# Kernel optimization log

Measured on AMD Instinct MI355X. Metric: run time of the kernel, lower is better.

Reference implementation:

```python
import jax, jax.numpy as jnp
import numpy as np


def setup_inputs() -> dict:
    key = jax.random.key(0)
    ks = jax.random.split(key, 6)
    B, L, H = 32, 2048, 1024
    return {
        "hidden_state": jax.random.normal(ks[0], (B, H), dtype=jnp.float32),
        "encoder_outputs": jax.random.normal(ks[1], (L, B, 2 * H), dtype=jnp.float32),
        "reduce_W": jax.random.normal(ks[2], (H, 2 * H), dtype=jnp.float32) * 0.02,
        "reduce_b": jax.random.normal(ks[3], (H,), dtype=jnp.float32) * 0.02,
        "attn_W": jax.random.normal(ks[4], (H, H), dtype=jnp.float32) * 0.02,
        "attn_b": jax.random.normal(ks[5], (H,), dtype=jnp.float32) * 0.02,
    }


def reference(hidden_state, encoder_outputs, reduce_W, reduce_b, attn_W, attn_b):
    # reduce_linear: [L, B, 2H] -> [L, B, H]
    reduced = jnp.einsum("lbk,hk->lbh", encoder_outputs, reduce_W) + reduce_b
    # 'general' score: dot(hidden_state[b], attn_linear(reduced[l, b]))
    proj = jnp.einsum("lbh,gh->lbg", reduced, attn_W) + attn_b  # [L, B, H]
    scores = jnp.einsum("bh,lbh->bl", hidden_state, proj)  # [B, L]
    return jax.nn.softmax(scores, axis=1)
```

## Files before the change

kernel.cpp:

```cpp
#include <hip/hip_runtime.h>

#define B 32
#define L 2048
#define H 1024
#define K2 2048
#define NL 8
#define HSPLIT 16
#define HCHUNK (H / HSPLIT)

__global__ __launch_bounds__(256) void v_kernel(const float* __restrict__ hs,
                                                const float* __restrict__ attn_W,
                                                float* __restrict__ v) {
    int tid = blockIdx.x * 256 + threadIdx.x;
    int b = tid >> 10;
    int h = tid & (H - 1);
    const float* hsb = hs + b * H;
    float acc = 0.f;
    #pragma unroll 8
    for (int g = 0; g < H; ++g)
        acc = fmaf(hsb[g], attn_W[g * H + h], acc);
    v[tid] = acc;
}

__global__ __launch_bounds__(256) void w_partial_kernel(const float* __restrict__ v,
                                                        const float* __restrict__ rW,
                                                        float* __restrict__ pw) {
    int k2 = blockIdx.x * 256 + threadIdx.x;
    int h0 = blockIdx.y * HCHUNK;
    const float2* rW2 = (const float2*)rW;
    float2 acc[B];
    #pragma unroll
    for (int b = 0; b < B; ++b) { acc[b].x = 0.f; acc[b].y = 0.f; }
    for (int h = h0; h < h0 + HCHUNK; ++h) {
        float2 rw = rW2[h * (K2 / 2) + k2];
        #pragma unroll
        for (int b = 0; b < B; ++b) {
            float vb = v[b * H + h];
            acc[b].x = fmaf(vb, rw.x, acc[b].x);
            acc[b].y = fmaf(vb, rw.y, acc[b].y);
        }
    }
    float2* pw2 = (float2*)pw;
    #pragma unroll
    for (int b = 0; b < B; ++b)
        pw2[(blockIdx.y * B + b) * (K2 / 2) + k2] = acc[b];
}

__global__ __launch_bounds__(256) void w_reduce_kernel(const float* __restrict__ pw,
                                                       float* __restrict__ w) {
    int i = blockIdx.x * 256 + threadIdx.x;
    float s = 0.f;
    #pragma unroll
    for (int p = 0; p < HSPLIT; ++p) s += pw[p * (B * K2) + i];
    w[i] = s;
}

__global__ __launch_bounds__(256) void scores_kernel(const float4* __restrict__ enc,
                                                     const float4* __restrict__ w,
                                                     float* __restrict__ scores) {
    int wid  = blockIdx.x * 4 + (threadIdx.x >> 6);
    int lane = threadIdx.x & 63;
    int b  = wid & (B - 1);
    int l0 = (wid >> 5) * NL;
    const float4* wb = w + b * (K2 / 4);
    float acc[NL];
    #pragma unroll
    for (int i = 0; i < NL; ++i) acc[i] = 0.f;
    for (int j = 0; j < (K2 / 4) / 64; ++j) {
        int idx = j * 64 + lane;
        float4 wv = wb[idx];
        #pragma unroll
        for (int i = 0; i < NL; ++i) {
            float4 e = enc[(size_t)((l0 + i) * B + b) * (K2 / 4) + idx];
            acc[i] = fmaf(wv.x, e.x, acc[i]);
            acc[i] = fmaf(wv.y, e.y, acc[i]);
            acc[i] = fmaf(wv.z, e.z, acc[i]);
            acc[i] = fmaf(wv.w, e.w, acc[i]);
        }
    }
    #pragma unroll
    for (int i = 0; i < NL; ++i) {
        float s = acc[i];
        #pragma unroll
        for (int off = 32; off > 0; off >>= 1) s += __shfl_down(s, off, 64);
        if (lane == 0) scores[b * L + l0 + i] = s;
    }
}

__global__ __launch_bounds__(256) void softmax_kernel(float* __restrict__ out) {
    int b = blockIdx.x;
    int t = threadIdx.x;
    float* row = out + b * L;
    float vals[8];
    float m = -3.4e38f;
    #pragma unroll
    for (int i = 0; i < 8; ++i) { vals[i] = row[t + i * 256]; m = fmaxf(m, vals[i]); }
    __shared__ float wred[4];
    int wv = t >> 6, lane = t & 63;
    #pragma unroll
    for (int off = 1; off < 64; off <<= 1) m = fmaxf(m, __shfl_xor(m, off, 64));
    if (lane == 0) wred[wv] = m;
    __syncthreads();
    m = fmaxf(fmaxf(wred[0], wred[1]), fmaxf(wred[2], wred[3]));
    __syncthreads();
    float s = 0.f;
    #pragma unroll
    for (int i = 0; i < 8; ++i) { vals[i] = __expf(vals[i] - m); s += vals[i]; }
    #pragma unroll
    for (int off = 1; off < 64; off <<= 1) s += __shfl_xor(s, off, 64);
    if (lane == 0) wred[wv] = s;
    __syncthreads();
    s = wred[0] + wred[1] + wred[2] + wred[3];
    float inv = 1.f / s;
    #pragma unroll
    for (int i = 0; i < 8; ++i) row[t + i * 256] = vals[i] * inv;
}

extern "C" void kernel_launch(void* const* d_in, const int* in_sizes, int n_in,
                              void* d_out, int out_size, void* d_ws, size_t ws_size,
                              hipStream_t stream) {
    const float* hs  = (const float*)d_in[0];
    const float* enc = (const float*)d_in[1];
    const float* rW  = (const float*)d_in[2];
    const float* aW  = (const float*)d_in[4];
    float* out = (float*)d_out;

    char* ws = (char*)d_ws;
    float* v  = (float*)(ws);
    float* w  = (float*)(ws + 131072);
    float* pw = (float*)(ws + 131072 + 262144);

    v_kernel<<<(B * H) / 256, 256, 0, stream>>>(hs, aW, v);

    dim3 g2(K2 / 512, HSPLIT);
    w_partial_kernel<<<g2, 256, 0, stream>>>(v, rW, pw);
    w_reduce_kernel<<<(B * K2) / 256, 256, 0, stream>>>(pw, w);

    scores_kernel<<<(L / NL) * B / 4, 256, 0, stream>>>((const float4*)enc,
                                                        (const float4*)w, out);
    softmax_kernel<<<B, 256, 0, stream>>>(out);
}
```

Measured before the change: 820.2 us.

## Replace split-H w reduction with direct per-output kernel and restructure scores per position

Merges the partial w computation and its reduction kernel into one kernel where each thread computes one full dot product over H, with more blocks and no partial buffer. Scores kernel is reorganized so each block handles one sequence position across all batches, streaming a contiguous encoder slab. The aim is to remove an extra launch and partial-sum traffic and to improve parallelism and access locality. In exchange, rW is re-read once per batch element, which leans on cache.

```diff
diff --git a/kernel.cpp b/kernel.cpp
--- a/kernel.cpp
+++ b/kernel.cpp
@@ -4,9 +4,6 @@
 #define L 2048
 #define H 1024
 #define K2 2048
-#define NL 8
-#define HSPLIT 16
-#define HCHUNK (H / HSPLIT)
 
 __global__ __launch_bounds__(256) void v_kernel(const float* __restrict__ hs,
                                                 const float* __restrict__ attn_W,
@@ -22,68 +19,51 @@
     v[tid] = acc;
 }
 
-__global__ __launch_bounds__(256) void w_partial_kernel(const float* __restrict__ v,
-                                                        const float* __restrict__ rW,
-                                                        float* __restrict__ pw) {
-    int k2 = blockIdx.x * 256 + threadIdx.x;
-    int h0 = blockIdx.y * HCHUNK;
-    const float2* rW2 = (const float2*)rW;
-    float2 acc[B];
-    #pragma unroll
-    for (int b = 0; b < B; ++b) { acc[b].x = 0.f; acc[b].y = 0.f; }
-    for (int h = h0; h < h0 + HCHUNK; ++h) {
-        float2 rw = rW2[h * (K2 / 2) + k2];
-        #pragma unroll
-        for (int b = 0; b < B; ++b) {
-            float vb = v[b * H + h];
-            acc[b].x = fmaf(vb, rw.x, acc[b].x);
-            acc[b].y = fmaf(vb, rw.y, acc[b].y);
-        }
-    }
-    float2* pw2 = (float2*)pw;
-    #pragma unroll
-    for (int b = 0; b < B; ++b)
-        pw2[(blockIdx.y * B + b) * (K2 / 2) + k2] = acc[b];
-}
-
-__global__ __launch_bounds__(256) void w_reduce_kernel(const float* __restrict__ pw,
-                                                       float* __restrict__ w) {
-    int i = blockIdx.x * 256 + threadIdx.x;
-    float s = 0.f;
-    #pragma unroll
-    for (int p = 0; p < HSPLIT; ++p) s += pw[p * (B * K2) + i];
-    w[i] = s;
+__global__ __launch_bounds__(256) void w_kernel(const float* __restrict__ v,
+                                                const float* __restrict__ rW,
+                                                float* __restrict__ w) {
+    int b = blockIdx.x >> 3;
+    int k = (blockIdx.x & 7) * 256 + threadIdx.x;
+    const float* vb = v + b * H;
+    float acc = 0.f;
+    #pragma unroll 8
+    for (int h = 0; h < H; ++h)
+        acc = fmaf(vb[h], rW[h * K2 + k], acc);
+    w[b * K2 + k] = acc;
 }
 
 __global__ __launch_bounds__(256) void scores_kernel(const float4* __restrict__ enc,
-                                                     const float4* __restrict__ w,
+                                                     const float4* __restrict__ w4,
                                                      float* __restrict__ scores) {
-    int wid  = blockIdx.x * 4 + (threadIdx.x >> 6);
-    int lane = threadIdx.x & 63;
-    int b  = wid & (B - 1);
-    int l0 = (wid >> 5) * NL;
-    const float4* wb = w + b * (K2 / 4);
-    float acc[NL];
+    const int l    = blockIdx.x;
+    const int wv   = threadIdx.x >> 6;
+    const int lane = threadIdx.x & 63;
+    const int b0   = wv * 8;
+    const float4* encl = enc + (size_t)l * (B * K2 / 4) + b0 * (K2 / 4);
+    const float4* wb0  = w4 + b0 * (K2 / 4);
+    float acc[8];
     #pragma unroll
-    for (int i = 0; i < NL; ++i) acc[i] = 0.f;
-    for (int j = 0; j < (K2 / 4) / 64; ++j) {
-        int idx = j * 64 + lane;
-        float4 wv = wb[idx];
+    for (int i = 0; i < 8; ++i) acc[i] = 0.f;
+    #pragma unroll
+    for (int i = 0; i < 8; ++i) {
+        const float4* e = encl + i * (K2 / 4);
+        const float4* wb = wb0 + i * (K2 / 4);
         #pragma unroll
-        for (int i = 0; i < NL; ++i) {
-            float4 e = enc[(size_t)((l0 + i) * B + b) * (K2 / 4) + idx];
-            acc[i] = fmaf(wv.x, e.x, acc[i]);
-            acc[i] = fmaf(wv.y, e.y, acc[i]);
-            acc[i] = fmaf(wv.z, e.z, acc[i]);
-            acc[i] = fmaf(wv.w, e.w, acc[i]);
+        for (int it = 0; it < 8; ++it) {
+            float4 ev = e[it * 64 + lane];
+            float4 wvv = wb[it * 64 + lane];
+            acc[i] = fmaf(ev.x, wvv.x, acc[i]);
+            acc[i] = fmaf(ev.y, wvv.y, acc[i]);
+            acc[i] = fmaf(ev.z, wvv.z, acc[i]);
+            acc[i] = fmaf(ev.w, wvv.w, acc[i]);
         }
     }
     #pragma unroll
-    for (int i = 0; i < NL; ++i) {
+    for (int i = 0; i < 8; ++i) {
         float s = acc[i];
         #pragma unroll
         for (int off = 32; off > 0; off >>= 1) s += __shfl_down(s, off, 64);
-        if (lane == 0) scores[b * L + l0 + i] = s;
+        if (lane == 0) scores[(b0 + i) * L + l] = s;
     }
 }
 
@@ -126,17 +106,11 @@
     float* out = (float*)d_out;
 
     char* ws = (char*)d_ws;
-    float* v  = (float*)(ws);
-    float* w  = (float*)(ws + 131072);
-    float* pw = (float*)(ws + 131072 + 262144);
+    float* v = (float*)(ws);
+    float* w = (float*)(ws + 131072);
 
     v_kernel<<<(B * H) / 256, 256, 0, stream>>>(hs, aW, v);
-
-    dim3 g2(K2 / 512, HSPLIT);
-    w_partial_kernel<<<g2, 256, 0, stream>>>(v, rW, pw);
-    w_reduce_kernel<<<(B * K2) / 256, 256, 0, stream>>>(pw, w);
-
-    scores_kernel<<<(L / NL) * B / 4, 256, 0, stream>>>((const float4*)enc,
-                                                        (const float4*)w, out);
+    w_kernel<<<(B * K2) / 256, 256, 0, stream>>>(v, rW, w);
+    scores_kernel<<<L, 256, 0, stream>>>((const float4*)enc, (const float4*)w, out);
     softmax_kernel<<<B, 256, 0, stream>>>(out);
 }
```

Measured after the change: 841.6 us. 2.6% more time.
